# Optimization experiments

Hardware: AMD Instinct MI355X
Metric: run time of the kernel (lower is better)

## Reference

```python
import jax, jax.numpy as jnp
import numpy as np

F = 15          # features
H = 128         # hidden_features
L = 12          # num_layers
NB = 16         # num_bins
M = 3 * NB - 1  # 47 params per feature (tails='linear')
TAIL = 3.0
MIN_W = 1e-3; MIN_H = 1e-3; MIN_D = 1e-3
B = 65536


def _masks():
    # nflows MADE sequential degrees
    deg_in = np.arange(1, F + 1)                       # input degrees 1..F
    deg_h = np.arange(H) % (F - 1) + 1                 # hidden degrees
    m_init = (deg_h[:, None] >= deg_in[None, :]).astype(np.float32)  # [H,F]
    m_h = (deg_h[:, None] >= deg_h[None, :]).astype(np.float32)      # [H,H]
    deg_out = np.repeat(deg_in, M)                     # tile -> repeat_interleave, [F*M]
    m_out = (deg_out[:, None] > deg_h[None, :]).astype(np.float32)   # [F*M,H], strict for output
    return jnp.asarray(m_init), jnp.asarray(m_h), jnp.asarray(m_out)


def setup_inputs() -> dict:
    key = jax.random.key(0)
    ks = jax.random.split(key, 7)
    s = 0.05
    return {
        "x": jax.random.normal(ks[0], (B, F), jnp.float32),
        "W_init": jax.random.normal(ks[1], (L, H, F), jnp.float32) * s,
        "b_init": jax.random.normal(ks[2], (L, H), jnp.float32) * s,
        "W_res": jax.random.normal(ks[3], (L, 2, 2, H, H), jnp.float32) * s,
        "b_res": jax.random.normal(ks[4], (L, 2, 2, H), jnp.float32) * s,
        "W_out": jax.random.normal(ks[5], (L, F * M, H), jnp.float32) * s,
        "b_out": jax.random.normal(ks[6], (L, F * M), jnp.float32) * s,
    }


def _made(x, p, m_init, m_h, m_out):
    # MADE with 2 masked residual blocks (relu, no BN/dropout), as in nflows
    h = x @ (p["W_init"] * m_init).T + p["b_init"]
    for blk in range(2):
        t = jax.nn.relu(h)
        t = t @ (p["W_res"][blk, 0] * m_h).T + p["b_res"][blk, 0]
        t = jax.nn.relu(t)
        t = t @ (p["W_res"][blk, 1] * m_h).T + p["b_res"][blk, 1]
        h = h + t
    return h @ (p["W_out"] * m_out).T + p["b_out"]  # [B, F*M]


def _rqs_forward(x, params):
    # unconstrained rational-quadratic spline, tails='linear' (nflows)
    uw = params[..., :NB]
    uh = params[..., NB:2 * NB]
    ud = params[..., 2 * NB:]                          # [B,F,NB-1]
    const = float(np.log(np.exp(1.0 - MIN_D) - 1.0))
    ud = jnp.pad(ud, ((0, 0), (0, 0), (1, 1)), constant_values=const)  # [B,F,NB+1]

    inside = (x >= -TAIL) & (x <= TAIL)
    xc = jnp.clip(x, -TAIL, TAIL)

    w = jax.nn.softmax(uw, axis=-1)
    w = MIN_W + (1.0 - MIN_W * NB) * w
    cw = jnp.pad(jnp.cumsum(w, axis=-1), ((0, 0), (0, 0), (1, 0)))
    cw = 2.0 * TAIL * cw - TAIL
    cw = cw.at[..., 0].set(-TAIL).at[..., -1].set(TAIL)
    w = cw[..., 1:] - cw[..., :-1]

    hgt = jax.nn.softmax(uh, axis=-1)
    hgt = MIN_H + (1.0 - MIN_H * NB) * hgt
    ch = jnp.pad(jnp.cumsum(hgt, axis=-1), ((0, 0), (0, 0), (1, 0)))
    ch = 2.0 * TAIL * ch - TAIL
    ch = ch.at[..., 0].set(-TAIL).at[..., -1].set(TAIL)
    hgt = ch[..., 1:] - ch[..., :-1]

    d = MIN_D + jax.nn.softplus(ud)                    # [B,F,NB+1]

    idx = jnp.clip(jnp.sum((xc[..., None] >= cw).astype(jnp.int32), axis=-1) - 1, 0, NB - 1)[..., None]
    g = lambda a: jnp.take_along_axis(a, idx, axis=-1)[..., 0]

    in_cw, in_w, in_ch, in_h = g(cw), g(w), g(ch), g(hgt)
    in_delta = g(hgt / w)
    in_d, in_d1 = g(d), g(d[..., 1:])

    theta = (xc - in_cw) / in_w
    tomt = theta * (1.0 - theta)
    num = in_h * (in_delta * theta ** 2 + in_d * tomt)
    den = in_delta + (in_d + in_d1 - 2.0 * in_delta) * tomt
    y = in_ch + num / den
    dnum = in_delta ** 2 * (in_d1 * theta ** 2 + 2.0 * in_delta * tomt + in_d * (1.0 - theta) ** 2)
    lad = jnp.log(dnum) - 2.0 * jnp.log(den)

    y = jnp.where(inside, y, x)                        # identity tails
    lad = jnp.where(inside, lad, 0.0)
    return y, jnp.sum(lad, axis=-1)


def reference(x, W_init, b_init, W_res, b_res, W_out, b_out):
    m_init, m_h, m_out = _masks()
    params = {"W_init": W_init, "b_init": b_init, "W_res": W_res,
              "b_res": b_res, "W_out": W_out, "b_out": b_out}

    def step(carry, p):
        xx, ld = carry
        xx = xx[:, ::-1]                               # ReversePermutation
        raw = _made(xx, p, m_init, m_h, m_out)
        xx, lad = _rqs_forward(xx, raw.reshape(xx.shape[0], F, M))
        return (xx, ld + lad), None

    (z, logdet), _ = jax.lax.scan(step, (x, jnp.zeros(x.shape[0], x.dtype)), params)
    return z, logdet
```

## Files before the change

kernel.cpp:

```cpp
#include <hip/hip_runtime.h>
#include <hip/hip_bf16.h>

#define FDIM 15
#define HDIM 128
#define LNUM 12
#define NBINS 16
#define MDIM 47
#define FM 705
#define BATCH 65536
#define TAILF 3.0f
#define MIN_Wc 0.001f
#define MIN_Hc 0.001f
#define MIN_Dc 0.001f

typedef __bf16 bf16_t;
typedef __attribute__((ext_vector_type(8))) __bf16 bf16x8;
typedef __attribute__((ext_vector_type(4))) __bf16 bf16x4;
typedef __attribute__((ext_vector_type(4))) float f32x4;

#define FRAGS_USED 211
#define FRAGS_PAD 224
#define FRAG_ELEMS 512
#define RING 16
#define WFRAG_TOTAL (LNUM * FRAGS_PAD * FRAG_ELEMS)

#define BB_FLOATS 1360
#define BB_TOTAL (LNUM * BB_FLOATS)

#define SPW 32

__device__ __forceinline__ int perm_pos(int pos) {
    int r, o;
    if (pos < 20) { r = pos / 10; o = pos % 10; }
    else          { r = 2 + (pos - 20) / 9; o = (pos - 20) % 9; }
    return r + 14 * o;
}

__device__ __forceinline__ float sp_softplus(float u) {
    return (u > 20.f) ? u : __logf(1.f + __expf(u));
}

__global__ void preproc_kernel(const float* __restrict__ Wi,
                               const float* __restrict__ Wr,
                               const float* __restrict__ Wo,
                               const float* __restrict__ bIg,
                               const float* __restrict__ bRg,
                               const float* __restrict__ bOg,
                               bf16_t* __restrict__ wfrag,
                               float* __restrict__ bblob) {
    const int RES_OFF[8] = {0, 1, 3, 5, 8, 11, 15, 19};
    const int OUT_OFF[15] = {0, 0, 3, 6, 9, 15, 21, 27, 36, 45, 54, 63, 75, 87, 99};
    const int OUT_CNT[15] = {0, 1, 1, 1, 2, 2, 2, 3, 3, 3, 3, 4, 4, 4, 4};

    int idx = blockIdx.x * blockDim.x + threadIdx.x;
    if (idx >= WFRAG_TOTAL) {
        int t = idx - WFRAG_TOTAL;
        if (t >= BB_TOTAL) return;
        int l = t / BB_FLOATS, r = t % BB_FLOATS;
        float v;
        if (r < 128) v = bIg[l * HDIM + perm_pos(r)];
        else if (r < 640) {
            int mat = (r - 128) >> 7, pos = (r - 128) & 127;
            v = bRg[(l * 4 + mat) * HDIM + perm_pos(pos)];
        } else {
            int q = r - 640, f = q / 48, j = q % 48;
            v = (j < 47) ? bOg[(size_t)l * FM + f * MDIM + j] : 0.f;
        }
        bblob[t] = v;
        return;
    }
    int j = idx & 7;
    int lane = (idx >> 3) & 63;
    int fg = idx >> 9;
    int g = fg % FRAGS_PAD;
    int l = fg / FRAGS_PAD;
    int quad = lane >> 4, n16 = lane & 15;
    int kk = quad * 8 + j;
    float val = 0.f;
    if (g < 8) {
        int n_orig = perm_pos(g * 16 + n16);
        if (kk < FDIM && (n_orig % 14) >= kk)
            val = Wi[(l * HDIM + n_orig) * FDIM + kk];
    } else if (g < 100) {
        int gg = g - 8;
        int mat = gg / 23, r = gg % 23;
        int mt = 7;
        while (mt > 0 && RES_OFF[mt] > r) mt--;
        int s = r - RES_OFF[mt];
        int j_orig = perm_pos(mt * 16 + n16);
        int k_orig = perm_pos(s * 32 + kk);
        if ((j_orig % 14) >= (k_orig % 14))
            val = Wr[((size_t)(l * 4 + mat) * HDIM + j_orig) * HDIM + k_orig];
    } else if (g < 211) {
        int gg = g - 100;
        int f = 14;
        while (f > 1 && OUT_OFF[f] > gg) f--;
        int q = gg - OUT_OFF[f];
        int cnt = OUT_CNT[f];
        int ty = q / cnt, s = q % cnt;
        int k_orig = perm_pos(s * 32 + kk);
        int o = (ty < 2) ? (f * MDIM + ty * 16 + n16)
                         : ((n16 < 15) ? (f * MDIM + 32 + n16) : -1);
        if (o >= 0 && f > (k_orig % 14))
            val = Wo[((size_t)l * FM + o) * HDIM + k_orig];
    }
    wfrag[idx] = (bf16_t)val;
}

__global__ __launch_bounds__(64, 2) void flow_kernel(
    const float* __restrict__ xin,
    float* __restrict__ zout,
    float* __restrict__ ldout,
    const bf16_t* __restrict__ wfrag,
    const float* __restrict__ bblob) {

    constexpr int RES_CNT_C[8] = {1, 2, 2, 3, 3, 4, 4, 4};
    constexpr int OUT_CNT_C[15] = {0, 1, 1, 1, 2, 2, 2, 3, 3, 3, 3, 4, 4, 4, 4};

    __shared__ __align__(16) float xs[SPW * 17];
    __shared__ __align__(16) unsigned char uni[13312];

    const int ln = threadIdx.x;
    const int quad = ln >> 4, n16 = ln & 15;
    const int fi = ln & 1, srow = ln >> 1;
    const int sbase = blockIdx.x * SPW;

    bf16_t* Bst = (bf16_t*)uni;
    float*  raw = (float*)uni;

    for (int t = ln; t < SPW * FDIM; t += 64) {
        int s = t / FDIM, c = t % FDIM;
        xs[s * 17 + c] = xin[(size_t)sbase * FDIM + t];
    }

    const bf16_t* wl = wfrag;
    bf16x8 Q[RING];
#pragma unroll
    for (int j = 0; j < RING; j++)
        Q[j] = *((const bf16x8*)(wl + (size_t)j * FRAG_ELEMS) + ln);

    float lad_sum = 0.f;
    bf16x8 bf[2][4];
    bf16x8 bfn[2][4];
    f32x4 h[2][8];

#pragma unroll 1
    for (int l = 0; l < LNUM; l++) {
        const float* bias = bblob + l * BB_FLOATS;

        float xc_pre[8];
#pragma unroll
        for (int p = 0; p < 8; p++) {
            int f = 2 * p + fi;
            xc_pre[p] = xs[srow * 17 + ((f < FDIM) ? (14 - f) : 0)];
        }
        bf16x8 a0[2];
#pragma unroll
        for (int T = 0; T < 2; T++)
#pragma unroll
            for (int j = 0; j < 8; j++) {
                int k = quad * 8 + j;
                a0[T][j] = (bf16_t)((k < FDIM) ? xs[(T * 16 + n16) * 17 + 14 - k] : 0.f);
            }

        int fp = 0;
        auto ldfrag = [&]() -> bf16x8 {
            bf16x8 r = Q[fp & (RING - 1)];
            Q[fp & (RING - 1)] =
                *((const bf16x8*)(wl + (size_t)(fp + RING) * FRAG_ELEMS) + ln);
            fp++;
            return r;
        };

        auto packmt = [&](int mt, f32x4 c0, f32x4 c1, bool relu) {
#pragma unroll
            for (int T = 0; T < 2; T++) {
                f32x4 c = T ? c1 : c0;
                bf16x4 pk;
#pragma unroll
                for (int r2 = 0; r2 < 4; r2++) {
                    float v = c[r2];
                    if (relu) v = fmaxf(v, 0.f);
                    pk[r2] = (bf16_t)v;
                }
                *(bf16x4*)&Bst[(T * 16 + n16) * 136 + mt * 16 + quad * 4] = pk;
            }
        };
        auto readpair = [&](int s2) {
#pragma unroll
            for (int T = 0; T < 2; T++)
                bfn[T][s2] = *(const bf16x8*)&Bst[(T * 16 + n16) * 136 + s2 * 32 + quad * 8];
        };
        auto commitbf = [&]() {
#pragma unroll
            for (int T = 0; T < 2; T++)
#pragma unroll
                for (int s = 0; s < 4; s++) bf[T][s] = bfn[T][s];
        };

#pragma unroll
        for (int mt = 0; mt < 8; mt++) {
            f32x4 bbv = *(const f32x4*)&bias[mt * 16 + quad * 4];
            bf16x8 wf = ldfrag();
            f32x4 c0 = __builtin_amdgcn_mfma_f32_16x16x32_bf16(wf, a0[0], bbv, 0, 0, 0);
            f32x4 c1 = __builtin_amdgcn_mfma_f32_16x16x32_bf16(wf, a0[1], bbv, 0, 0, 0);
            h[0][mt] = c0; h[1][mt] = c1;
            packmt(mt, c0, c1, true);
            if (mt & 1) readpair(mt >> 1);
        }
        commitbf();

        auto gemm_pack = [&](const float* bm, bool addto, bool relu) {
#pragma unroll
            for (int mt = 0; mt < 8; mt++) {
                f32x4 bbv = *(const f32x4*)&bm[mt * 16 + quad * 4];
                f32x4 acc0 = addto ? (h[0][mt] + bbv) : bbv;
                f32x4 acc1 = addto ? (h[1][mt] + bbv) : bbv;
#pragma unroll
                for (int s = 0; s < RES_CNT_C[mt]; s++) {
                    bf16x8 wf = ldfrag();
                    acc0 = __builtin_amdgcn_mfma_f32_16x16x32_bf16(wf, bf[0][s], acc0, 0, 0, 0);
                    acc1 = __builtin_amdgcn_mfma_f32_16x16x32_bf16(wf, bf[1][s], acc1, 0, 0, 0);
                }
                if (addto) { h[0][mt] = acc0; h[1][mt] = acc1; }
                packmt(mt, acc0, acc1, relu);
                if (mt & 1) readpair(mt >> 1);
            }
            commitbf();
        };

        gemm_pack(bias + 128 + 0 * HDIM, false, true);
        gemm_pack(bias + 128 + 1 * HDIM, true,  true);
        gemm_pack(bias + 128 + 2 * HDIM, false, true);
        gemm_pack(bias + 128 + 3 * HDIM, true,  false);

        const float* bO48 = bias + 640;

#pragma unroll
        for (int p = 0; p < 8; p++) {
            const int nf = (p < 7) ? 2 : 1;
#pragma unroll
            for (int ff = 0; ff < 2; ff++) {
                if (ff >= nf) break;
                const int f = 2 * p + ff;
                const int cnt = OUT_CNT_C[f];
#pragma unroll
                for (int ty = 0; ty < 3; ty++) {
                    f32x4 acc0 = *(const f32x4*)&bO48[f * 48 + ty * 16 + quad * 4];
                    f32x4 acc1 = acc0;
#pragma unroll
                    for (int s = 0; s < cnt; s++) {
                        bf16x8 wf = ldfrag();
                        acc0 = __builtin_amdgcn_mfma_f32_16x16x32_bf16(wf, bf[0][s], acc0, 0, 0, 0);
                        acc1 = __builtin_amdgcn_mfma_f32_16x16x32_bf16(wf, bf[1][s], acc1, 0, 0, 0);
                    }
                    *(f32x4*)&raw[(ff * 32 + n16) * 52 + ty * 16 + quad * 4] = acc0;
                    *(f32x4*)&raw[(ff * 32 + 16 + n16) * 52 + ty * 16 + quad * 4] = acc1;
                }
            }

            if (fi < nf) {
                int f = 2 * p + fi;
                const float* rp = &raw[(fi * 32 + srow) * 52];
                float xr = xc_pre[p];
                bool inside = (xr >= -TAILF) && (xr <= TAILF);
                float xcv = fminf(fmaxf(xr, -TAILF), TAILF);

                float uw[NBINS], uh[NBINS], dv[NBINS];
                {
                    f32x4 v0 = *(const f32x4*)(rp + 0);
                    f32x4 v1 = *(const f32x4*)(rp + 4);
                    f32x4 v2 = *(const f32x4*)(rp + 8);
                    f32x4 v3 = *(const f32x4*)(rp + 12);
                    f32x4 w0 = *(const f32x4*)(rp + 16);
                    f32x4 w1 = *(const f32x4*)(rp + 20);
                    f32x4 w2 = *(const f32x4*)(rp + 24);
                    f32x4 w3 = *(const f32x4*)(rp + 28);
                    f32x4 e0 = *(const f32x4*)(rp + 32);
                    f32x4 e1 = *(const f32x4*)(rp + 36);
                    f32x4 e2 = *(const f32x4*)(rp + 40);
                    f32x4 e3 = *(const f32x4*)(rp + 44);
#pragma unroll
                    for (int i = 0; i < 4; i++) {
                        uw[i] = v0[i]; uw[4 + i] = v1[i]; uw[8 + i] = v2[i]; uw[12 + i] = v3[i];
                        uh[i] = w0[i]; uh[4 + i] = w1[i]; uh[8 + i] = w2[i]; uh[12 + i] = w3[i];
                        dv[i] = e0[i]; dv[4 + i] = e1[i]; dv[8 + i] = e2[i]; dv[12 + i] = e3[i];
                    }
                }

                float ew[NBINS], eh[NBINS];
#pragma unroll
                for (int i = 0; i < NBINS; i++) {
                    ew[i] = __expf(uw[i]);
                    eh[i] = __expf(uh[i]);
                }
                float swv, shv;
                {
                    float s0 = ew[0] + ew[1], s1 = ew[2] + ew[3];
                    float s2 = ew[4] + ew[5], s3 = ew[6] + ew[7];
                    float s4 = ew[8] + ew[9], s5 = ew[10] + ew[11];
                    float s6 = ew[12] + ew[13], s7 = ew[14] + ew[15];
                    swv = ((s0 + s1) + (s2 + s3)) + ((s4 + s5) + (s6 + s7));
                    float t0 = eh[0] + eh[1], t1 = eh[2] + eh[3];
                    float t2 = eh[4] + eh[5], t3 = eh[6] + eh[7];
                    float t4 = eh[8] + eh[9], t5 = eh[10] + eh[11];
                    float t6 = eh[12] + eh[13], t7 = eh[14] + eh[15];
                    shv = ((t0 + t1) + (t2 + t3)) + ((t4 + t5) + (t6 + t7));
                }

                const float mwc2 = 2.f * TAILF * MIN_Wc;
                float isw2 = (2.f * TAILF) * (1.f - NBINS * MIN_Wc) * __builtin_amdgcn_rcpf(swv);
                float ish2 = (2.f * TAILF) * (1.f - NBINS * MIN_Hc) * __builtin_amdgcn_rcpf(shv);
                float wb2[NBINS], hb2[NBINS];
#pragma unroll
                for (int i = 0; i < NBINS; i++) {
                    wb2[i] = fmaf(ew[i], isw2, mwc2);
                    hb2[i] = fmaf(eh[i], ish2, mwc2);
                }

                float cwr = -TAILF, chr = -TAILF;
                float lw = -TAILF, chl = -TAILF;
                float curw = wb2[0], curh = hb2[0];
                float d0r = dv[0], d1r = dv[0];
                bool gt0 = false, lt15 = true;
#pragma unroll
                for (int b = 0; b < NBINS - 1; b++) {
                    cwr += wb2[b]; chr += hb2[b];
                    bool v = (xcv >= cwr);
                    if (b == 0) gt0 = v;
                    if (b == NBINS - 2) lt15 = !v;
                    lw   = v ? cwr : lw;
                    chl  = v ? chr : chl;
                    curw = v ? wb2[b + 1] : curw;
                    curh = v ? hb2[b + 1] : curh;
                    d0r  = v ? dv[b] : d0r;
                    d1r  = v ? dv[b + 1] : d1r;
                }

                float spl0 = sp_softplus(d0r), spl1 = sp_softplus(d1r);
                float d0 = gt0 ? (MIN_Dc + spl0) : 1.f;
                float d1 = lt15 ? (MIN_Dc + spl1) : 1.f;

                float rw = __builtin_amdgcn_rcpf(curw);
                float delta = curh * rw;
                float th = (xcv - lw) * rw;
                float omt = 1.f - th;
                float tomt = th * omt;
                float num = curh * (delta * th * th + d0 * tomt);
                float den = delta + (d0 + d1 - 2.f * delta) * tomt;
                float rd = __builtin_amdgcn_rcpf(den);
                float y = chl + num * rd;
                float dnum = delta * delta * (d1 * th * th + 2.f * delta * tomt + d0 * omt * omt);
                float lad = 0.69314718055994531f * __log2f(dnum * rd * rd);

                y = inside ? y : xr;
                lad = inside ? lad : 0.f;
                xs[srow * 17 + f] = y;
                lad_sum += lad;
            }
        }

#pragma unroll
        for (int d = 0; d < FRAGS_PAD - FRAGS_USED; d++) {
            (void)ldfrag();
        }

        wl += (size_t)FRAGS_PAD * FRAG_ELEMS;
    }

    float v = lad_sum;
    v += __shfl_xor(v, 1);
    if (fi == 0) ldout[(size_t)sbase + srow] = v;

    for (int t = ln; t < SPW * FDIM; t += 64) {
        int s = t / FDIM, c = t % FDIM;
        zout[(size_t)sbase * FDIM + t] = xs[s * 17 + c];
    }
}

extern "C" void kernel_launch(void* const* d_in, const int* in_sizes, int n_in,
                              void* d_out, int out_size, void* d_ws, size_t ws_size,
                              hipStream_t stream) {
    const float* x  = (const float*)d_in[0];
    const float* Wi = (const float*)d_in[1];
    const float* bI = (const float*)d_in[2];
    const float* Wr = (const float*)d_in[3];
    const float* bR = (const float*)d_in[4];
    const float* Wo = (const float*)d_in[5];
    const float* bO = (const float*)d_in[6];

    bf16_t* wfrag = (bf16_t*)d_ws;
    size_t woff = ((size_t)WFRAG_TOTAL * 2 + (size_t)RING * FRAG_ELEMS * 2 + 255) & ~(size_t)255;
    float* bblob = (float*)((char*)d_ws + woff);
    float* zout  = (float*)d_out;
    float* ldout_final = zout + (size_t)BATCH * FDIM;

    const int totalP = WFRAG_TOTAL + BB_TOTAL;
    preproc_kernel<<<(totalP + 255) / 256, 256, 0, stream>>>(Wi, Wr, Wo, bI, bR, bO, wfrag, bblob);

    flow_kernel<<<BATCH / SPW, 64, 0, stream>>>(x, zout, ldout_final, wfrag, bblob);
}
```

Baseline: 373.1 us.

## Prefetch biases one stage ahead and fold log2e into output weights

Bias vectors for each GEMM stage and the output-layer biases are now loaded into registers one stage earlier, including across layer boundaries, so global bias loads overlap the MFMA work. The output weights and biases are pre-scaled by log2(e) in preprocessing so the spline can use exp2 directly instead of exp. The softplus overflow guard is removed. This adds register pressure, and both the missing guard and bf16 rounding of the scaled weights could shift numerics slightly.

```diff
diff --git a/kernel.cpp b/kernel.cpp
--- a/kernel.cpp
+++ b/kernel.cpp
@@ -12,6 +12,8 @@
 #define MIN_Wc 0.001f
 #define MIN_Hc 0.001f
 #define MIN_Dc 0.001f
+#define LOG2E 1.4426950408889634f
+#define LN2 0.69314718055994531f
 
 typedef __bf16 bf16_t;
 typedef __attribute__((ext_vector_type(8))) __bf16 bf16x8;
@@ -34,10 +36,6 @@
     if (pos < 20) { r = pos / 10; o = pos % 10; }
     else          { r = 2 + (pos - 20) / 9; o = (pos - 20) % 9; }
     return r + 14 * o;
-}
-
-__device__ __forceinline__ float sp_softplus(float u) {
-    return (u > 20.f) ? u : __logf(1.f + __expf(u));
 }
 
 __global__ void preproc_kernel(const float* __restrict__ Wi,
@@ -64,7 +62,7 @@
             v = bRg[(l * 4 + mat) * HDIM + perm_pos(pos)];
         } else {
             int q = r - 640, f = q / 48, j = q % 48;
-            v = (j < 47) ? bOg[(size_t)l * FM + f * MDIM + j] : 0.f;
+            v = (j < 47) ? bOg[(size_t)l * FM + f * MDIM + j] * LOG2E : 0.f;
         }
         bblob[t] = v;
         return;
@@ -102,7 +100,7 @@
         int o = (ty < 2) ? (f * MDIM + ty * 16 + n16)
                          : ((n16 < 15) ? (f * MDIM + 32 + n16) : -1);
         if (o >= 0 && f > (k_orig % 14))
-            val = Wo[((size_t)l * FM + o) * HDIM + k_orig];
+            val = Wo[((size_t)l * FM + o) * HDIM + k_orig] * LOG2E;
     }
     wfrag[idx] = (bf16_t)val;
 }
@@ -139,6 +137,17 @@
     for (int j = 0; j < RING; j++)
         Q[j] = *((const bf16x8*)(wl + (size_t)j * FRAG_ELEMS) + ln);
 
+    f32x4 bb[8];
+#pragma unroll
+    for (int mt = 0; mt < 8; mt++)
+        bb[mt] = *(const f32x4*)&bblob[mt * 16 + quad * 4];
+    f32x4 ob[6];
+#pragma unroll
+    for (int j = 0; j < 6; j++) {
+        int ff = j / 3, ty = j % 3;
+        ob[j] = *(const f32x4*)&bblob[640 + ff * 48 + ty * 16 + quad * 4];
+    }
+
     float lad_sum = 0.f;
     bf16x8 bf[2][4];
     bf16x8 bfn[2][4];
@@ -147,6 +156,9 @@
 #pragma unroll 1
     for (int l = 0; l < LNUM; l++) {
         const float* bias = bblob + l * BB_FLOATS;
+        const float* nbias = bblob + ((l < LNUM - 1) ? (l + 1) : (LNUM - 1)) * BB_FLOATS;
+        const float* bO48 = bias + 640;
+        const float* nb648 = nbias + 640;
 
         float xc_pre[8];
 #pragma unroll
@@ -200,7 +212,8 @@
 
 #pragma unroll
         for (int mt = 0; mt < 8; mt++) {
-            f32x4 bbv = *(const f32x4*)&bias[mt * 16 + quad * 4];
+            f32x4 bbv = bb[mt];
+            bb[mt] = *(const f32x4*)&bias[128 + 0 * HDIM + mt * 16 + quad * 4];
             bf16x8 wf = ldfrag();
             f32x4 c0 = __builtin_amdgcn_mfma_f32_16x16x32_bf16(wf, a0[0], bbv, 0, 0, 0);
             f32x4 c1 = __builtin_amdgcn_mfma_f32_16x16x32_bf16(wf, a0[1], bbv, 0, 0, 0);
@@ -210,10 +223,11 @@
         }
         commitbf();
 
-        auto gemm_pack = [&](const float* bm, bool addto, bool relu) {
+        auto gemm_pack = [&](const float* bm_next, bool addto, bool relu) {
 #pragma unroll
             for (int mt = 0; mt < 8; mt++) {
-                f32x4 bbv = *(const f32x4*)&bm[mt * 16 + quad * 4];
+                f32x4 bbv = bb[mt];
+                bb[mt] = *(const f32x4*)&bm_next[mt * 16 + quad * 4];
                 f32x4 acc0 = addto ? (h[0][mt] + bbv) : bbv;
                 f32x4 acc1 = addto ? (h[1][mt] + bbv) : bbv;
 #pragma unroll
@@ -229,12 +243,10 @@
             commitbf();
         };
 
-        gemm_pack(bias + 128 + 0 * HDIM, false, true);
-        gemm_pack(bias + 128 + 1 * HDIM, true,  true);
-        gemm_pack(bias + 128 + 2 * HDIM, false, true);
-        gemm_pack(bias + 128 + 3 * HDIM, true,  false);
-
-        const float* bO48 = bias + 640;
+        gemm_pack(bias + 128 + 1 * HDIM, false, true);
+        gemm_pack(bias + 128 + 2 * HDIM, true,  true);
+        gemm_pack(bias + 128 + 3 * HDIM, false, true);
+        gemm_pack(nbias,                 true,  false);
 
 #pragma unroll
         for (int p = 0; p < 8; p++) {
@@ -246,7 +258,13 @@
                 const int cnt = OUT_CNT_C[f];
 #pragma unroll
                 for (int ty = 0; ty < 3; ty++) {
-                    f32x4 acc0 = *(const f32x4*)&bO48[f * 48 + ty * 16 + quad * 4];
+                    f32x4 acc0 = ob[ff * 3 + ty];
+                    {
+                        const float* rbase = (p == 7) ? nb648 : bO48;
+                        int fr = (p == 7) ? ff : (2 * (p + 1) + ff);
+                        if (fr > 14) fr = 14;
+                        ob[ff * 3 + ty] = *(const f32x4*)&rbase[fr * 48 + ty * 16 + quad * 4];
+                    }
                     f32x4 acc1 = acc0;
 #pragma unroll
                     for (int s = 0; s < cnt; s++) {
@@ -257,6 +275,11 @@
                     *(f32x4*)&raw[(ff * 32 + n16) * 52 + ty * 16 + quad * 4] = acc0;
                     *(f32x4*)&raw[(ff * 32 + 16 + n16) * 52 + ty * 16 + quad * 4] = acc1;
                 }
+            }
+            if (p == 7) {
+#pragma unroll
+                for (int ty2 = 0; ty2 < 3; ty2++)
+                    ob[3 + ty2] = *(const f32x4*)&nb648[1 * 48 + ty2 * 16 + quad * 4];
             }
 
             if (fi < nf) {
@@ -291,8 +314,8 @@
                 float ew[NBINS], eh[NBINS];
 #pragma unroll
                 for (int i = 0; i < NBINS; i++) {
-                    ew[i] = __expf(uw[i]);
-                    eh[i] = __expf(uh[i]);
+                    ew[i] = __builtin_exp2f(uw[i]);
+                    eh[i] = __builtin_exp2f(uh[i]);
                 }
                 float swv, shv;
                 {
@@ -337,7 +360,8 @@
                     d1r  = v ? dv[b + 1] : d1r;
                 }
 
-                float spl0 = sp_softplus(d0r), spl1 = sp_softplus(d1r);
+                float spl0 = LN2 * __log2f(1.f + __builtin_exp2f(d0r));
+                float spl1 = LN2 * __log2f(1.f + __builtin_exp2f(d1r));
                 float d0 = gt0 ? (MIN_Dc + spl0) : 1.f;
                 float d1 = lt15 ? (MIN_Dc + spl1) : 1.f;
 
@@ -351,7 +375,7 @@
                 float rd = __builtin_amdgcn_rcpf(den);
                 float y = chl + num * rd;
                 float dnum = delta * delta * (d1 * th * th + 2.f * delta * tomt + d0 * omt * omt);
-                float lad = 0.69314718055994531f * __log2f(dnum * rd * rd);
+                float lad = LN2 * __log2f(dnum * rd * rd);
 
                 y = inside ? y : xr;
                 lad = inside ? lad : 0.f;
```

Result: slower. 413.4 us (+10.8%).
